# Kernel tuning notes

Measured on AMD Instinct MI355X. Metric: run time of the kernel, lower is better.

The kernel has to match this reference:

```python
import jax, jax.numpy as jnp
import numpy as np

EPS = 1e-6
B, N, M, C, H = 4, 2048, 1024, 1024, 16
HD = C // H          # 64
HID = 4 * C          # 4096
SCALE = 1.0 / np.sqrt(HD)


def _ln(x, g, b):
    m = x.mean(-1, keepdims=True)
    v = jnp.mean((x - m) ** 2, -1, keepdims=True)
    return (x - m) * jax.lax.rsqrt(v + EPS) * g + b


def _rot(x):
    # interleaved rotate: (-x2, x1) pairs (rotate_half=False path)
    x1, x2 = x[..., ::2], x[..., 1::2]
    return jnp.stack([-x2, x1], axis=-1).reshape(x.shape)


def _apply_rope(x, emb):
    # emb: [N, 2*HD] = cat(sin, cos); x: [B,H,N,HD]
    sin, cos = jnp.split(emb, 2, axis=-1)
    return x * cos + _rot(x) * sin


def _sdpa(q, k, v):
    s = jnp.einsum('bhqd,bhkd->bhqk', q, k) * SCALE
    a = jax.nn.softmax(s, axis=-1)
    return jnp.einsum('bhqk,bhkd->bhqd', a, v)


def _forward(x, ctx, rope,
             wqkv, sa_qg, sa_qb, sa_kg, sa_kb, sa_wo, sa_bo,
             ca_wq, ca_wk, ca_wv, ca_qg, ca_qb, ca_kg, ca_kb, ca_wo, ca_bo, ca_gate,
             w1g, b1g, w1x, b1x, w2, b2, ls0, ls1, ls2):
    Bx, Nx, Cx = x.shape
    Mx = ctx.shape[1]
    # ---- self attention (fused QKV, qk-norm, RoPE) ----
    qkv = (x @ wqkv).reshape(Bx, Nx, 3, H, HD).transpose(2, 0, 3, 1, 4)  # [3,B,H,N,HD]
    q, k, v = qkv[0], qkv[1], qkv[2]
    q = _ln(q, sa_qg, sa_qb)
    k = _ln(k, sa_kg, sa_kb)
    q = _apply_rope(q, rope)
    k = _apply_rope(k, rope)
    sa = _sdpa(q, k, v).transpose(0, 2, 1, 3).reshape(Bx, Nx, Cx)
    sa = sa @ sa_wo + sa_bo
    x = ls0 * sa + x
    # ---- cross attention (GQA degenerate: n_kv_heads == n_q_heads), gated ----
    q = (x @ ca_wq).reshape(Bx, Nx, H, HD).transpose(0, 2, 1, 3)
    k = (ctx @ ca_wk).reshape(Bx, Mx, H, HD).transpose(0, 2, 1, 3)
    v = (ctx @ ca_wv).reshape(Bx, Mx, H, HD).transpose(0, 2, 1, 3)
    q = _ln(q, ca_qg, ca_qb)
    k = _ln(k, ca_kg, ca_kb)
    q = _apply_rope(q, rope)  # rope on queries only; ctx has its own positions
    ca = _sdpa(q, k, v).transpose(0, 2, 1, 3).reshape(Bx, Nx, Cx)
    ca = (ca @ ca_wo + ca_bo) * jnp.tanh(ca_gate)
    x = ls1 * ca + x
    # ---- SwiGLU FFN ----
    h = jax.nn.silu(x @ w1g + b1g) * (x @ w1x + b1x)
    f = h @ w2 + b2
    x = ls2 * f + x
    return x


def setup_inputs() -> dict:
    key = jax.random.key(0)
    ks = iter(jax.random.split(key, 32))
    rn = lambda shape, s=0.02: (jax.random.normal(next(ks), shape, jnp.float32) * s)
    inp = {
        'x': jax.random.normal(next(ks), (B, N, C), jnp.float32),
        'ctx': jax.random.normal(next(ks), (B, M, C), jnp.float32),
    }
    # rotary table: cat(sin, cos), interleaved-repeated freqs -> [N, 2*HD]
    pos = jnp.arange(N, dtype=jnp.float32)
    inv = 1.0 / (10000.0 ** (jnp.arange(0, HD, 2, dtype=jnp.float32) / HD))
    ang = pos[:, None] * inv[None, :]                      # [N, HD/2]
    sin = jnp.repeat(jnp.sin(ang), 2, axis=-1)
    cos = jnp.repeat(jnp.cos(ang), 2, axis=-1)
    inp['rope'] = jnp.concatenate([sin, cos], axis=-1)
    inp.update(
        wqkv=rn((C, 3 * C)),
        sa_qg=jnp.ones((HD,)), sa_qb=jnp.zeros((HD,)),
        sa_kg=jnp.ones((HD,)), sa_kb=jnp.zeros((HD,)),
        sa_wo=rn((C, C)), sa_bo=jnp.zeros((C,)),
        ca_wq=rn((C, C)), ca_wk=rn((C, C)), ca_wv=rn((C, C)),
        ca_qg=jnp.ones((HD,)), ca_qb=jnp.zeros((HD,)),
        ca_kg=jnp.ones((HD,)), ca_kb=jnp.zeros((HD,)),
        ca_wo=rn((C, C)), ca_bo=jnp.zeros((C,)),
        ca_gate=jnp.full((C,), 0.5, jnp.float32),
        w1g=rn((C, HID)), b1g=jnp.zeros((HID,)),
        w1x=rn((C, HID)), b1x=jnp.zeros((HID,)),
        w2=rn((HID, C)), b2=jnp.zeros((C,)),
        ls0=jnp.full((C,), 1e-5, jnp.float32),
        ls1=jnp.full((C,), 1e-5, jnp.float32),
        ls2=jnp.full((C,), 1e-5, jnp.float32),
    )
    return inp


def reference(x, ctx, rope,
              wqkv, sa_qg, sa_qb, sa_kg, sa_kb, sa_wo, sa_bo,
              ca_wq, ca_wk, ca_wv, ca_qg, ca_qb, ca_kg, ca_kb, ca_wo, ca_bo, ca_gate,
              w1g, b1g, w1x, b1x, w2, b2, ls0, ls1, ls2):
    return _forward(x, ctx, rope,
                    wqkv, sa_qg, sa_qb, sa_kg, sa_kb, sa_wo, sa_bo,
                    ca_wq, ca_wk, ca_wv, ca_qg, ca_qb, ca_kg, ca_kb, ca_wo, ca_bo, ca_gate,
                    w1g, b1g, w1x, b1x, w2, b2, ls0, ls1, ls2)
```

## Files before the change

### kernel.cpp

```cpp
#include <hip/hip_runtime.h>
#include <hip/hip_bf16.h>
#include <math.h>


typedef __attribute__((ext_vector_type(8))) short bf16x8;
typedef __attribute__((ext_vector_type(4))) short s16x4;
typedef __attribute__((ext_vector_type(4))) float f32x4;

#define DEV __device__ __forceinline__

DEV unsigned short f2us(float f) {
  __hip_bfloat16 h = __float2bfloat16(f);
  return __builtin_bit_cast(unsigned short, h);
}

DEV void gload_lds16(const void* g, void* l) {
  __builtin_amdgcn_global_load_lds((const __attribute__((address_space(1))) void*)g,
                                   (__attribute__((address_space(3))) void*)l, 16, 0, 0);
}

#define MFMA_BF16_16x16x32 __builtin_amdgcn_mfma_f32_16x16x32_bf16
#define WAITV0 asm volatile("s_waitcnt vmcnt(0)" ::: "memory")


__global__ __launch_bounds__(256) void cvt_f32_bf16(const float* __restrict__ in,
                                                    __hip_bfloat16* __restrict__ out,
                                                    long n) {
  long i = ((long)blockIdx.x * blockDim.x + threadIdx.x) * 4;
  if (i + 3 < n) {
    float4 v = *(const float4*)(in + i);
    out[i + 0] = __float2bfloat16(v.x);
    out[i + 1] = __float2bfloat16(v.y);
    out[i + 2] = __float2bfloat16(v.z);
    out[i + 3] = __float2bfloat16(v.w);
  }
}

__global__ __launch_bounds__(256) void transpose_cvt(const float* __restrict__ w,
                                                     __hip_bfloat16* __restrict__ wT,
                                                     int K, int N) {
  __shared__ float tile[32][33];
  int n0 = blockIdx.x * 32, k0 = blockIdx.y * 32;
  int tx = threadIdx.x, ty = threadIdx.y;
  #pragma unroll
  for (int i = 0; i < 32; i += 8)
    tile[ty + i][tx] = w[(long)(k0 + ty + i) * N + n0 + tx];
  __syncthreads();
  #pragma unroll
  for (int i = 0; i < 32; i += 8)
    wT[(long)(n0 + ty + i) * K + k0 + tx] = __float2bfloat16(tile[tx][ty + i]);
}

__global__ __launch_bounds__(256) void transpose_cvt_ilv(const float* __restrict__ w,
                                                         __hip_bfloat16* __restrict__ wI,
                                                         int K, int N, int ofs) {
  __shared__ float tile[32][33];
  int n0 = blockIdx.x * 32, k0 = blockIdx.y * 32;
  int tx = threadIdx.x, ty = threadIdx.y;
  #pragma unroll
  for (int i = 0; i < 32; i += 8)
    tile[ty + i][tx] = w[(long)(k0 + ty + i) * N + n0 + tx];
  __syncthreads();
  #pragma unroll
  for (int i = 0; i < 32; i += 8) {
    int j = n0 + ty + i;
    int r = 32 * (j >> 4) + (j & 15) + ofs;
    wI[(long)r * K + k0 + tx] = __float2bfloat16(tile[tx][ty + i]);
  }
}

template <int EPI>
DEV void epi_store(long idx, long col, float v,
                   float* __restrict__ out_f, __hip_bfloat16* __restrict__ out_b,
                   const float* __restrict__ bias, const float* __restrict__ scale,
                   const float* __restrict__ gate, const float* __restrict__ resid,
                   const __hip_bfloat16* __restrict__ mulin) {
  if constexpr (EPI == 0) {
    out_b[idx] = __float2bfloat16(v);
  } else if constexpr (EPI == 1) {
    float r = scale[col] * (v + bias[col]) + resid[idx];
    out_b[idx] = __float2bfloat16(r);
  } else if constexpr (EPI == 2) {
    float r = scale[col] * ((v + bias[col]) * tanhf(gate[col])) + __bfloat162float(mulin[idx]);
    out_b[idx] = __float2bfloat16(r);
  } else {
    out_f[idx] = scale[col] * (v + bias[col]) + __bfloat162float(mulin[idx]);
  }
}

template <int BM, int EPI>
__global__ __launch_bounds__(512, 2) void gemm2ph(const __hip_bfloat16* __restrict__ A,
                                                  const __hip_bfloat16* __restrict__ Bt,
                                                  int M, int N, int K,
                                                  float* __restrict__ out_f,
                                                  __hip_bfloat16* __restrict__ out_b,
                                                  const float* __restrict__ bias,
                                                  const float* __restrict__ scale,
                                                  const float* __restrict__ gate,
                                                  const float* __restrict__ resid,
                                                  const __hip_bfloat16* __restrict__ mulin) {
  constexpr int MF = BM / 32;
  constexpr int WRS = BM / 2;
  constexpr int AJ = BM * 8 / 512;
  __shared__ __align__(16) unsigned short As[2][BM * 64];
  __shared__ __align__(16) unsigned short Bs[2][256 * 64];

  int t = threadIdx.x;
  int l = t & 63, w = t >> 6;
  int lo = l & 15, hi = l >> 4;
  int wr = w >> 2, wc = w & 3;
  long bm = blockIdx.x, bn = blockIdx.y;
  const __hip_bfloat16* Ab = A + bm * BM * (long)K;
  const __hip_bfloat16* Bb = Bt + bn * 256 * (long)K;
  int nt = K >> 6;

  auto stage = [&](int kt, int buf) {
    long kb = (long)kt * 64;
    #pragma unroll
    for (int j = 0; j < AJ; j++) {
      int q = j * 512 + t;
      int row = q >> 3, c = (q & 7) ^ (row & 7);
      gload_lds16(Ab + (long)row * K + kb + c * 8, &As[buf][q * 8]);
    }
    #pragma unroll
    for (int j = 0; j < 4; j++) {
      int q = j * 512 + t;
      int row = q >> 3, c = (q & 7) ^ (row & 7);
      gload_lds16(Bb + (long)row * K + kb + c * 8, &Bs[buf][q * 8]);
    }
  };

  f32x4 acc[MF][4] = {};

  stage(0, 0);
  WAITV0;
  __builtin_amdgcn_s_barrier();

  for (int kt = 0; kt < nt; ++kt) {
    int cur = kt & 1;
    if (kt + 1 < nt) stage(kt + 1, cur ^ 1);

    #pragma unroll
    for (int ks = 0; ks < 2; ks++) {
      bf16x8 bfrag[4];
      #pragma unroll
      for (int n = 0; n < 4; n++) {
        int rb = wc * 64 + n * 16 + lo;
        bfrag[n] = *(const bf16x8*)&Bs[cur][rb * 64 + (((ks << 2) | hi) ^ (rb & 7)) * 8];
      }
      #pragma unroll
      for (int mg = 0; mg < MF; mg += 4) {
        bf16x8 afrag[4];
        #pragma unroll
        for (int m = 0; m < 4; m++) {
          int ra = wr * WRS + (mg + m) * 16 + lo;
          afrag[m] = *(const bf16x8*)&As[cur][ra * 64 + (((ks << 2) | hi) ^ (ra & 7)) * 8];
        }
        __builtin_amdgcn_s_setprio(1);
        #pragma unroll
        for (int m = 0; m < 4; m++)
          #pragma unroll
          for (int n = 0; n < 4; n++)
            acc[mg + m][n] = MFMA_BF16_16x16x32(afrag[m], bfrag[n], acc[mg + m][n], 0, 0, 0);
        __builtin_amdgcn_s_setprio(0);
      }
    }

    if (kt + 1 < nt) {
      WAITV0;
      __builtin_amdgcn_s_barrier();
    }
  }

  if constexpr (EPI == 6) {
    #pragma unroll
    for (int m = 0; m < MF; m++)
      #pragma unroll
      for (int np = 0; np < 2; np++)
        #pragma unroll
        for (int i = 0; i < 4; i++) {
          long row = bm * BM + wr * WRS + m * 16 + hi * 4 + i;
          long jc = bn * 128 + wc * 32 + np * 16 + lo;
          float g = acc[m][np * 2][i] + bias[jc];
          float xv = acc[m][np * 2 + 1][i] + gate[jc];
          float hv = (g / (1.f + expf(-g))) * xv;
          out_b[row * (long)(N >> 1) + jc] = __float2bfloat16(hv);
        }
  } else if constexpr (EPI == 8 || EPI == 9 || EPI == 10) {
    int colbase = (int)(bn * 256 + wc * 64);
    int slice = colbase >> 10;
    bool dovt = (EPI == 8 && slice == 2) || (EPI == 10 && slice == 1);
    if (dovt) {
      unsigned short* vt = (unsigned short*)mulin;
      int h = (colbase >> 6) & 15;
      int kvt_in_b = (EPI == 8) ? ((int)(bm & 15) * 2 + wr) : ((int)(bm & 7) * 2 + wr);
      constexpr int NTV = (EPI == 8) ? 32 : 16;
      #pragma unroll
      for (int m = 0; m < MF; m++) {
        long row0 = bm * BM + wr * WRS + m * 16 + hi * 4;
        int b = (int)(row0 >> ((EPI == 8) ? 11 : 10));
        long base = ((long)(b * 16 + h) * NTV + kvt_in_b) * 4608 + (m * 16 + hi * 4);
        #pragma unroll
        for (int nn = 0; nn < 4; nn++) {
          s16x4 pw;
          pw[0] = (short)f2us(acc[m][nn][0]);
          pw[1] = (short)f2us(acc[m][nn][1]);
          pw[2] = (short)f2us(acc[m][nn][2]);
          pw[3] = (short)f2us(acc[m][nn][3]);
          *(s16x4*)&vt[base + (nn * 16 + lo) * 72] = pw;
        }
      }
    } else {
      bool doln;
      const float *gv_p, *bv_p;
      if constexpr (EPI == 8) {
        doln = true;
        gv_p = (slice == 0) ? bias : gate;
        bv_p = (slice == 0) ? scale : resid;
      } else if constexpr (EPI == 9) {
        doln = true; gv_p = bias; bv_p = scale;
      } else {
        doln = true; gv_p = bias; bv_p = scale;
      }
      bool dorope = (EPI == 8) || (EPI == 9);
      if (EPI == 8 && slice == 1) dorope = true;
      (void)doln;
      float gv[4], bv[4];
      #pragma unroll
      for (int nn = 0; nn < 4; nn++) {
        gv[nn] = gv_p[nn * 16 + lo];
        bv[nn] = bv_p[nn * 16 + lo];
      }
      #pragma unroll
      for (int m = 0; m < MF; m++)
        #pragma unroll
        for (int i = 0; i < 4; i++) {
          float v0 = acc[m][0][i], v1 = acc[m][1][i], v2 = acc[m][2][i], v3 = acc[m][3][i];
          float s = (v0 + v1) + (v2 + v3);
          s += __shfl_xor(s, 1); s += __shfl_xor(s, 2);
          s += __shfl_xor(s, 4); s += __shfl_xor(s, 8);
          float mean = s * 0.015625f;
          float d0 = v0 - mean, d1 = v1 - mean, d2 = v2 - mean, d3 = v3 - mean;
          float q2 = (d0 * d0 + d1 * d1) + (d2 * d2 + d3 * d3);
          q2 += __shfl_xor(q2, 1); q2 += __shfl_xor(q2, 2);
          q2 += __shfl_xor(q2, 4); q2 += __shfl_xor(q2, 8);
          float rstd = rsqrtf(q2 * 0.015625f + 1e-6f);
          long row = bm * BM + wr * WRS + m * 16 + hi * 4 + i;
          int nseq = (int)(row & 2047);
          float xsv[4] = {d0 * rstd, d1 * rstd, d2 * rstd, d3 * rstd};
          #pragma unroll
          for (int nn = 0; nn < 4; nn++) {
            float xn = xsv[nn] * gv[nn] + bv[nn];
            if constexpr (EPI != 10) {
              float partner = __shfl_xor(xn, 1);
              int d = nn * 16 + lo;
              float sn = out_f[(long)nseq * 128 + d];
              float cs = out_f[(long)nseq * 128 + 64 + d];
              xn = (lo & 1) ? (xn * cs + partner * sn) : (xn * cs - partner * sn);
            }
            out_b[row * (long)N + colbase + nn * 16 + lo] = __float2bfloat16(xn);
          }
        }
    }
  } else {
    #pragma unroll
    for (int m = 0; m < MF; m++)
      #pragma unroll
      for (int n = 0; n < 4; n++)
        #pragma unroll
        for (int i = 0; i < 4; i++) {
          long row = bm * BM + wr * WRS + m * 16 + hi * 4 + i;
          long col = bn * 256 + wc * 64 + n * 16 + lo;
          epi_store<EPI>(row * (long)N + col, col, acc[m][n][i],
                         out_f, out_b, bias, scale, gate, resid, mulin);
        }
  }
}

__global__ __launch_bounds__(256) void attn32(const __hip_bfloat16* __restrict__ qB, long qBatch, long qRow,
                                              const __hip_bfloat16* __restrict__ kB, long kBatch, long kRow,
                                              const __hip_bfloat16* __restrict__ vt,
                                              __hip_bfloat16* __restrict__ out, int Nq, int Nkv) {
  const float SC2 = 0.125f * 1.44269504089f;
  int t = threadIdx.x;
  int l = t & 63, w = t >> 6;
  int lo = l & 15, hi = l >> 4;
  int nQC = Nq >> 7;
  int qc = blockIdx.x % nQC;
  int bh = blockIdx.x / nQC;
  int h = bh & 15, b = bh >> 4;
  int q0 = qc * 128 + w * 32;

  __shared__ unsigned short P_all[4][32 * 72];
  __shared__ unsigned short V_lds[2][64 * 72];
  unsigned short* P = P_all[w];

  bf16x8 qf[2][2];
#pragma unroll
  for (int qs = 0; qs < 2; qs++) {
    const __hip_bfloat16* qp = qB + (long)b * qBatch + (long)(q0 + qs * 16 + lo) * qRow + h * 64 + hi * 8;
    qf[qs][0] = *(const bf16x8*)qp;
    qf[qs][1] = *(const bf16x8*)(qp + 32);
  }

  float mrow[2] = {-INFINITY, -INFINITY};
  float lsum[2] = {0.f, 0.f};
  f32x4 acc[2][4] = {};
  const f32x4 fz = {0.f, 0.f, 0.f, 0.f};

  const __hip_bfloat16* kbase = kB + (long)b * kBatch + h * 64 + hi * 8;
  int nt = Nkv >> 6;
  const char* vtb = (const char*)vt + (long)bh * nt * 9216;

  auto stageV = [&](int tile, unsigned short* dstb) {
    const char* src = vtb + (long)tile * 9216;
    gload_lds16(src + t * 16, &dstb[t * 8]);
    gload_lds16(src + (t + 256) * 16, &dstb[(t + 256) * 8]);
    if (t < 64) gload_lds16(src + (t + 512) * 16, &dstb[(t + 512) * 8]);
  };
  auto loadK = [&](int tile, bf16x8 (&kg)[4][2]) {
#pragma unroll
    for (int g = 0; g < 4; g++) {
      const __hip_bfloat16* kp = kbase + (long)(tile * 64 + g * 16 + lo) * kRow;
      kg[g][0] = *(const bf16x8*)kp;
      kg[g][1] = *(const bf16x8*)(kp + 32);
    }
  };
  auto qkt = [&](bf16x8 (&kg)[4][2], f32x4 (&ST)[2][4]) {
    __builtin_amdgcn_s_setprio(1);
#pragma unroll
    for (int qs = 0; qs < 2; qs++)
#pragma unroll
      for (int g = 0; g < 4; g++) {
        f32x4 s0 = MFMA_BF16_16x16x32(kg[g][0], qf[qs][0], fz, 0, 0, 0);
        ST[qs][g] = MFMA_BF16_16x16x32(kg[g][1], qf[qs][1], s0, 0, 0, 0);
      }
    __builtin_amdgcn_s_setprio(0);
  };
  auto smax = [&](f32x4 (&ST)[2][4]) {
#pragma unroll
    for (int qs = 0; qs < 2; qs++) {
      float mg0 = fmaxf(fmaxf(ST[qs][0][0], ST[qs][0][1]), fmaxf(ST[qs][0][2], ST[qs][0][3]));
      float mg1 = fmaxf(fmaxf(ST[qs][1][0], ST[qs][1][1]), fmaxf(ST[qs][1][2], ST[qs][1][3]));
      float mg2 = fmaxf(fmaxf(ST[qs][2][0], ST[qs][2][1]), fmaxf(ST[qs][2][2], ST[qs][2][3]));
      float mg3 = fmaxf(fmaxf(ST[qs][3][0], ST[qs][3][1]), fmaxf(ST[qs][3][2], ST[qs][3][3]));
      float rm = fmaxf(fmaxf(mg0, mg1), fmaxf(mg2, mg3)) * SC2;
      rm = fmaxf(rm, __shfl_xor(rm, 16));
      rm = fmaxf(rm, __shfl_xor(rm, 32));
      if (!__all(rm <= mrow[qs] + 8.f)) {
        float mn = fmaxf(mrow[qs], rm);
        float scl = exp2f(mrow[qs] - mn);
        mrow[qs] = mn;
        lsum[qs] *= scl;
        float c0 = __shfl(scl, hi * 4 + 0);
        float c1 = __shfl(scl, hi * 4 + 1);
        float c2 = __shfl(scl, hi * 4 + 2);
        float c3 = __shfl(scl, hi * 4 + 3);
#pragma unroll
        for (int tt = 0; tt < 4; tt++) {
          acc[qs][tt][0] *= c0; acc[qs][tt][1] *= c1;
          acc[qs][tt][2] *= c2; acc[qs][tt][3] *= c3;
        }
      }
      float m = mrow[qs];
      float rs = 0.f;
#pragma unroll
      for (int g = 0; g < 4; g++) {
        float p0 = exp2f(fmaf(ST[qs][g][0], SC2, -m));
        float p1 = exp2f(fmaf(ST[qs][g][1], SC2, -m));
        float p2 = exp2f(fmaf(ST[qs][g][2], SC2, -m));
        float p3 = exp2f(fmaf(ST[qs][g][3], SC2, -m));
        rs += (p0 + p1) + (p2 + p3);
        s16x4 pw;
        pw[0] = (short)f2us(p0); pw[1] = (short)f2us(p1);
        pw[2] = (short)f2us(p2); pw[3] = (short)f2us(p3);
        *(s16x4*)&P[(qs * 16 + lo) * 72 + g * 16 + hi * 4] = pw;
      }
      rs += __shfl_xor(rs, 16);
      rs += __shfl_xor(rs, 32);
      lsum[qs] += rs;
    }
  };
  auto pv = [&](const unsigned short* Vb) {
    bf16x8 pf[2][2];
#pragma unroll
    for (int qs = 0; qs < 2; qs++) {
      pf[qs][0] = *(const bf16x8*)&P[(qs * 16 + lo) * 72 + hi * 8];
      pf[qs][1] = *(const bf16x8*)&P[(qs * 16 + lo) * 72 + 32 + hi * 8];
    }
    __builtin_amdgcn_s_setprio(1);
#pragma unroll
    for (int tt = 0; tt < 4; tt++) {
      bf16x8 v0 = *(const bf16x8*)&Vb[(tt * 16 + lo) * 72 + hi * 8];
      bf16x8 v1 = *(const bf16x8*)&Vb[(tt * 16 + lo) * 72 + 32 + hi * 8];
#pragma unroll
      for (int qs = 0; qs < 2; qs++) {
        acc[qs][tt] = MFMA_BF16_16x16x32(pf[qs][0], v0, acc[qs][tt], 0, 0, 0);
        acc[qs][tt] = MFMA_BF16_16x16x32(pf[qs][1], v1, acc[qs][tt], 0, 0, 0);
      }
    }
    __builtin_amdgcn_s_setprio(0);
  };

  bf16x8 kgA[4][2], kgB[4][2];
  stageV(0, V_lds[0]);
  loadK(0, kgA);

  for (int it = 0; it < nt; it += 2) {
    __syncthreads();
    stageV(it + 1, V_lds[1]);
    f32x4 ST0[2][4];
    qkt(kgA, ST0);
    loadK(it + 1, kgB);
    smax(ST0);
    pv(V_lds[0]);

    __syncthreads();
    if (it + 2 < nt) stageV(it + 2, V_lds[0]);
    f32x4 ST1[2][4];
    qkt(kgB, ST1);
    if (it + 2 < nt) loadK(it + 2, kgA);
    smax(ST1);
    pv(V_lds[1]);
  }

#pragma unroll
  for (int qs = 0; qs < 2; qs++) {
    float inv = 1.f / lsum[qs];
    float iv0 = __shfl(inv, hi * 4 + 0);
    float iv1 = __shfl(inv, hi * 4 + 1);
    float iv2 = __shfl(inv, hi * 4 + 2);
    float iv3 = __shfl(inv, hi * 4 + 3);
    float iv[4] = {iv0, iv1, iv2, iv3};
#pragma unroll
    for (int i = 0; i < 4; i++) {
      long row = q0 + qs * 16 + hi * 4 + i;
      __hip_bfloat16* op = out + ((long)b * Nq + row) * 1024 + h * 64 + lo;
#pragma unroll
      for (int tt = 0; tt < 4; tt++) op[tt * 16] = __float2bfloat16(acc[qs][tt][i] * iv[i]);
    }
  }
}


extern "C" void kernel_launch(void* const* d_in, const int* in_sizes, int n_in,
                              void* d_out, int out_size, void* d_ws, size_t ws_size,
                              hipStream_t stream) {
  (void)in_sizes; (void)n_in; (void)out_size; (void)ws_size;

  const float* x      = (const float*)d_in[0];
  const float* ctx    = (const float*)d_in[1];
  const float* rope   = (const float*)d_in[2];
  const float* wqkv   = (const float*)d_in[3];
  const float* sa_qg  = (const float*)d_in[4];
  const float* sa_qb  = (const float*)d_in[5];
  const float* sa_kg  = (const float*)d_in[6];
  const float* sa_kb  = (const float*)d_in[7];
  const float* sa_wo  = (const float*)d_in[8];
  const float* sa_bo  = (const float*)d_in[9];
  const float* ca_wq  = (const float*)d_in[10];
  const float* ca_wk  = (const float*)d_in[11];
  const float* ca_wv  = (const float*)d_in[12];
  const float* ca_qg  = (const float*)d_in[13];
  const float* ca_qb  = (const float*)d_in[14];
  const float* ca_kg  = (const float*)d_in[15];
  const float* ca_kb  = (const float*)d_in[16];
  const float* ca_wo  = (const float*)d_in[17];
  const float* ca_bo  = (const float*)d_in[18];
  const float* ca_gate= (const float*)d_in[19];
  const float* w1g    = (const float*)d_in[20];
  const float* b1g    = (const float*)d_in[21];
  const float* w1x    = (const float*)d_in[22];
  const float* b1x    = (const float*)d_in[23];
  const float* w2     = (const float*)d_in[24];
  const float* b2     = (const float*)d_in[25];
  const float* ls0    = (const float*)d_in[26];
  const float* ls1    = (const float*)d_in[27];
  const float* ls2    = (const float*)d_in[28];

  char* ws = (char*)d_ws;

  const long OFF_WQKVT = 0;
  const long OFF_SAWOT = 6291456;
  const long OFF_CAWQT = 8388608;
  const long OFF_CAWKT = 10485760;
  const long OFF_CAWVT = 12582912;
  const long OFF_CAWOT = 14680064;
  const long OFF_W1I   = 16777216;
  const long OFF_W2T   = 33554432;
  const long OFF_XB    = 41943040;
  const long OFF_QC    = OFF_XB;
  const long OFF_CTXB  = 58720256;
  const long OFF_QKV   = 67108864;
  const long OFF_CAO   = 67108864;
  const long OFF_X2B   = 83886080;
  const long OFF_SG    = 100663296;
  const long OFF_SAO   = 117440512;
  const long OFF_KVC   = 117440512;
  const long OFF_CAVT  = 134217728;
  const long OFF_X1B   = 167772160;
  const long OFF_SAVT  = 184549376;

  auto bfp = [&](long off) { return (__hip_bfloat16*)(ws + off); };

  dim3 tb32(32, 8);
  transpose_cvt<<<dim3(96, 32), tb32, 0, stream>>>(wqkv,  bfp(OFF_WQKVT), 1024, 3072);
  transpose_cvt<<<dim3(32, 32), tb32, 0, stream>>>(sa_wo, bfp(OFF_SAWOT), 1024, 1024);
  transpose_cvt<<<dim3(32, 32), tb32, 0, stream>>>(ca_wq, bfp(OFF_CAWQT), 1024, 1024);
  transpose_cvt<<<dim3(32, 32), tb32, 0, stream>>>(ca_wk, bfp(OFF_CAWKT), 1024, 1024);
  transpose_cvt<<<dim3(32, 32), tb32, 0, stream>>>(ca_wv, bfp(OFF_CAWVT), 1024, 1024);
  transpose_cvt<<<dim3(32, 32), tb32, 0, stream>>>(ca_wo, bfp(OFF_CAWOT), 1024, 1024);
  transpose_cvt_ilv<<<dim3(128, 32), tb32, 0, stream>>>(w1g, bfp(OFF_W1I), 1024, 4096, 0);
  transpose_cvt_ilv<<<dim3(128, 32), tb32, 0, stream>>>(w1x, bfp(OFF_W1I), 1024, 4096, 16);
  transpose_cvt<<<dim3(32, 128), tb32, 0, stream>>>(w2,   bfp(OFF_W2T), 4096, 1024);

  cvt_f32_bf16<<<8192, 256, 0, stream>>>(x,   bfp(OFF_XB),   8388608);
  cvt_f32_bf16<<<4096, 256, 0, stream>>>(ctx, bfp(OFF_CTXB), 4194304);

  gemm2ph<128, 8><<<dim3(64, 12), 512, 0, stream>>>(bfp(OFF_XB), bfp(OFF_WQKVT), 8192, 3072, 1024,
                                                    (float*)rope, bfp(OFF_QKV),
                                                    sa_qg, sa_qb, sa_kg, sa_kb, bfp(OFF_SAVT));

  attn32<<<1024, 256, 0, stream>>>(bfp(OFF_QKV),        (long)2048 * 3072, 3072,
                                   bfp(OFF_QKV) + 1024, (long)2048 * 3072, 3072,
                                   bfp(OFF_SAVT), bfp(OFF_SAO), 2048, 2048);

  gemm2ph<128, 1><<<dim3(64, 4), 512, 0, stream>>>(bfp(OFF_SAO), bfp(OFF_SAWOT), 8192, 1024, 1024,
                                                   nullptr, bfp(OFF_X1B), sa_bo, ls0, nullptr, x, nullptr);

  gemm2ph<128, 9><<<dim3(64, 4), 512, 0, stream>>>(bfp(OFF_X1B), bfp(OFF_CAWQT), 8192, 1024, 1024,
                                                   (float*)rope, bfp(OFF_QC),
                                                   ca_qg, ca_qb, nullptr, nullptr, nullptr);
  gemm2ph<128, 10><<<dim3(32, 8), 512, 0, stream>>>(bfp(OFF_CTXB), bfp(OFF_CAWKT), 4096, 2048, 1024,
                                                    nullptr, bfp(OFF_KVC),
                                                    ca_kg, ca_kb, nullptr, nullptr, bfp(OFF_CAVT));

  attn32<<<1024, 256, 0, stream>>>(bfp(OFF_QC), (long)2048 * 1024, 1024,
                                   bfp(OFF_KVC), (long)1024 * 2048, 2048,
                                   bfp(OFF_CAVT), bfp(OFF_CAO), 2048, 1024);

  gemm2ph<128, 2><<<dim3(64, 4), 512, 0, stream>>>(bfp(OFF_CAO), bfp(OFF_CAWOT), 8192, 1024, 1024,
                                                   nullptr, bfp(OFF_X2B), ca_bo, ls1, ca_gate, nullptr,
                                                   bfp(OFF_X1B));

  gemm2ph<256, 6><<<dim3(32, 32), 512, 0, stream>>>(bfp(OFF_X2B), bfp(OFF_W1I), 8192, 8192, 1024,
                                                    nullptr, bfp(OFF_SG), b1g, nullptr, b1x, nullptr, nullptr);

  gemm2ph<128, 5><<<dim3(64, 4), 512, 0, stream>>>(bfp(OFF_SG), bfp(OFF_W2T), 8192, 1024, 4096,
                                                   (float*)d_out, nullptr, b2, ls2, nullptr, nullptr,
                                                   bfp(OFF_X2B));
}
```

Measured before the change: 737.9 us.

## Swizzle P and V^T LDS layouts instead of padding; truncate P to bf16

Replaces the 72-element padded row layout for the attention P scratch and the pre-transposed V tiles with an unpadded 64-element layout that uses an XOR swizzle of 8-element chunks. The GEMM epilogue writes V^T directly in the swizzled layout, so each V tile is 8 KB and is staged with two LDS DMA loads per thread instead of three. The goal is fewer staging instructions, less LDS usage and less global traffic while still avoiding bank conflicts. It also converts P to bf16 by truncation rather than rounding, which is cheaper but slightly biases the probabilities downward.

```diff
diff --git a/kernel.cpp b/kernel.cpp
--- a/kernel.cpp
+++ b/kernel.cpp
@@ -12,6 +12,10 @@
 DEV unsigned short f2us(float f) {
   __hip_bfloat16 h = __float2bfloat16(f);
   return __builtin_bit_cast(unsigned short, h);
+}
+
+DEV short f2us_trunc(float f) {
+  return (short)(__builtin_bit_cast(unsigned, f) >> 16);
 }
 
 DEV void gload_lds16(const void* g, void* l) {
@@ -193,38 +197,36 @@
     if (dovt) {
       unsigned short* vt = (unsigned short*)mulin;
       int h = (colbase >> 6) & 15;
-      int kvt_in_b = (EPI == 8) ? ((int)(bm & 15) * 2 + wr) : ((int)(bm & 7) * 2 + wr);
+      int kvt = (EPI == 8) ? ((int)(bm & 15) * 2 + wr) : ((int)(bm & 7) * 2 + wr);
       constexpr int NTV = (EPI == 8) ? 32 : 16;
       #pragma unroll
       for (int m = 0; m < MF; m++) {
         long row0 = bm * BM + wr * WRS + m * 16 + hi * 4;
         int b = (int)(row0 >> ((EPI == 8) ? 11 : 10));
-        long base = ((long)(b * 16 + h) * NTV + kvt_in_b) * 4608 + (m * 16 + hi * 4);
+        long tb = ((long)(b * 16 + h) * NTV + kvt) * 4096;
+        int gk = 2 * m + (hi >> 1);
         #pragma unroll
         for (int nn = 0; nn < 4; nn++) {
+          int drow = nn * 16 + lo;
           s16x4 pw;
           pw[0] = (short)f2us(acc[m][nn][0]);
           pw[1] = (short)f2us(acc[m][nn][1]);
           pw[2] = (short)f2us(acc[m][nn][2]);
           pw[3] = (short)f2us(acc[m][nn][3]);
-          *(s16x4*)&vt[base + (nn * 16 + lo) * 72] = pw;
+          long off = tb + (long)drow * 64 + (((gk ^ (drow & 7)) << 3) | ((hi & 1) << 2));
+          *(s16x4*)&vt[off] = pw;
         }
       }
     } else {
-      bool doln;
       const float *gv_p, *bv_p;
       if constexpr (EPI == 8) {
-        doln = true;
         gv_p = (slice == 0) ? bias : gate;
         bv_p = (slice == 0) ? scale : resid;
       } else if constexpr (EPI == 9) {
-        doln = true; gv_p = bias; bv_p = scale;
+        gv_p = bias; bv_p = scale;
       } else {
-        doln = true; gv_p = bias; bv_p = scale;
-      }
-      bool dorope = (EPI == 8) || (EPI == 9);
-      if (EPI == 8 && slice == 1) dorope = true;
-      (void)doln;
+        gv_p = bias; bv_p = scale;
+      }
       float gv[4], bv[4];
       #pragma unroll
       for (int nn = 0; nn < 4; nn++) {
@@ -291,8 +293,8 @@
   int h = bh & 15, b = bh >> 4;
   int q0 = qc * 128 + w * 32;
 
-  __shared__ unsigned short P_all[4][32 * 72];
-  __shared__ unsigned short V_lds[2][64 * 72];
+  __shared__ unsigned short P_all[4][32 * 64];
+  __shared__ unsigned short V_lds[2][64 * 64];
   unsigned short* P = P_all[w];
 
   bf16x8 qf[2][2];
@@ -310,13 +312,12 @@
 
   const __hip_bfloat16* kbase = kB + (long)b * kBatch + h * 64 + hi * 8;
   int nt = Nkv >> 6;
-  const char* vtb = (const char*)vt + (long)bh * nt * 9216;
+  const char* vtb = (const char*)vt + (long)bh * nt * 8192;
 
   auto stageV = [&](int tile, unsigned short* dstb) {
-    const char* src = vtb + (long)tile * 9216;
+    const char* src = vtb + (long)tile * 8192;
     gload_lds16(src + t * 16, &dstb[t * 8]);
     gload_lds16(src + (t + 256) * 16, &dstb[(t + 256) * 8]);
-    if (t < 64) gload_lds16(src + (t + 512) * 16, &dstb[(t + 512) * 8]);
   };
   auto loadK = [&](int tile, bf16x8 (&kg)[4][2]) {
 #pragma unroll
@@ -364,6 +365,8 @@
       }
       float m = mrow[qs];
       float rs = 0.f;
+      int qrow = qs * 16 + lo;
+      int sw = lo & 7;
 #pragma unroll
       for (int g = 0; g < 4; g++) {
         float p0 = exp2f(fmaf(ST[qs][g][0], SC2, -m));
@@ -372,9 +375,10 @@
         float p3 = exp2f(fmaf(ST[qs][g][3], SC2, -m));
         rs += (p0 + p1) + (p2 + p3);
         s16x4 pw;
-        pw[0] = (short)f2us(p0); pw[1] = (short)f2us(p1);
-        pw[2] = (short)f2us(p2); pw[3] = (short)f2us(p3);
-        *(s16x4*)&P[(qs * 16 + lo) * 72 + g * 16 + hi * 4] = pw;
+        pw[0] = f2us_trunc(p0); pw[1] = f2us_trunc(p1);
+        pw[2] = f2us_trunc(p2); pw[3] = f2us_trunc(p3);
+        int gk = 2 * g + (hi >> 1);
+        *(s16x4*)&P[qrow * 64 + (((gk ^ sw) << 3) | ((hi & 1) << 2))] = pw;
       }
       rs += __shfl_xor(rs, 16);
       rs += __shfl_xor(rs, 32);
@@ -383,16 +387,19 @@
   };
   auto pv = [&](const unsigned short* Vb) {
     bf16x8 pf[2][2];
+    int sw = lo & 7;
 #pragma unroll
     for (int qs = 0; qs < 2; qs++) {
-      pf[qs][0] = *(const bf16x8*)&P[(qs * 16 + lo) * 72 + hi * 8];
-      pf[qs][1] = *(const bf16x8*)&P[(qs * 16 + lo) * 72 + 32 + hi * 8];
+      int qrow = qs * 16 + lo;
+      pf[qs][0] = *(const bf16x8*)&P[qrow * 64 + ((hi ^ sw) << 3)];
+      pf[qs][1] = *(const bf16x8*)&P[qrow * 64 + (((4 | hi) ^ sw) << 3)];
     }
     __builtin_amdgcn_s_setprio(1);
 #pragma unroll
     for (int tt = 0; tt < 4; tt++) {
-      bf16x8 v0 = *(const bf16x8*)&Vb[(tt * 16 + lo) * 72 + hi * 8];
-      bf16x8 v1 = *(const bf16x8*)&Vb[(tt * 16 + lo) * 72 + 32 + hi * 8];
+      int drow = tt * 16 + lo;
+      bf16x8 v0 = *(const bf16x8*)&Vb[drow * 64 + ((hi ^ sw) << 3)];
+      bf16x8 v1 = *(const bf16x8*)&Vb[drow * 64 + (((4 | hi) ^ sw) << 3)];
 #pragma unroll
       for (int qs = 0; qs < 2; qs++) {
         acc[qs][tt] = MFMA_BF16_16x16x32(pf[qs][0], v0, acc[qs][tt], 0, 0, 0);
```

New measurement: 724.8 us (median of 2 runs). No clear change (-1.8%).
